# Performance work log

Hardware: AMD Instinct MI355X
Metric: run time of the kernel (lower is better)

## Reference

```python
import jax, jax.numpy as jnp
import numpy as np

BATCH_SIZE = 4
TEMPERATURE = 0.07
NEG_MASK_VAL = -10.0


def setup_inputs() -> dict:
    key = jax.random.key(0)
    k1, k2 = jax.random.split(key)
    N, D = 16384, 256  # N = batch_size * n_patches
    feat_q = jax.random.normal(k1, (N, D), dtype=jnp.float32)
    feat_k = jax.random.normal(k2, (N, D), dtype=jnp.float32)
    return {"feat_q": feat_q, "feat_k": feat_k}


def reference(feat_q, feat_k):
    N, d = feat_q.shape
    feat_k = jax.lax.stop_gradient(feat_k)  # detach
    # positive logits: dot of matching rows -> [N, 1]
    l_pos = jnp.einsum('nd,nd->n', feat_q, feat_k)[:, None]
    q = feat_q.reshape(BATCH_SIZE, -1, d)  # [B, P, D]
    k = feat_k.reshape(BATCH_SIZE, -1, d)
    P = q.shape[1]
    # intra-batch-element negatives: [B, P, P]
    l_neg = jnp.einsum('bpd,bqd->bpq', q, k)
    eye = jnp.eye(P, dtype=bool)[None, :, :]
    l_neg = jnp.where(eye, jnp.float32(NEG_MASK_VAL), l_neg).reshape(-1, P)
    out = jnp.concatenate([l_pos, l_neg], axis=1) / TEMPERATURE  # [N, 1+P]
    # cross-entropy with target class 0, reduction='none'
    loss = -jax.nn.log_softmax(out, axis=1)[:, 0]
    return loss
```

## Files before the change

### kernel.cpp

```cpp
#include <hip/hip_runtime.h>
#include <hip/hip_bf16.h>


typedef __attribute__((ext_vector_type(8))) short short8;
typedef __attribute__((ext_vector_type(4))) float f32x4;

#define BATCH 4
#define PN 4096
#define DD 256
#define NP (BATCH * PN)

constexpr float kLog2e = 1.4426950408889634f;
constexpr float kScale = kLog2e / 0.07f;
constexpr float kMask2 = -10.0f * kScale;
constexpr float kLn2   = 0.6931471805599453f;
constexpr float kNegInf = -3.0e38f;

__device__ __forceinline__ unsigned short f2bf(float f) {
  __hip_bfloat16 h = __float2bfloat16(f);
  return *reinterpret_cast<unsigned short*>(&h);
}

__device__ __forceinline__ float fexp2(float x) {
#if __has_builtin(__builtin_amdgcn_exp2f)
  return __builtin_amdgcn_exp2f(x);
#else
  return exp2f(x);
#endif
}
__device__ __forceinline__ float flog2(float x) {
#if __has_builtin(__builtin_amdgcn_logf)
  return __builtin_amdgcn_logf(x);
#else
  return log2f(x);
#endif
}

__global__ void k_convert(const float* __restrict__ src,
                          unsigned short* __restrict__ dst, int n4) {
  int i = blockIdx.x * blockDim.x + threadIdx.x;
  if (i >= n4) return;
  float4 v = reinterpret_cast<const float4*>(src)[i];
  ushort4 o;
  o.x = f2bf(v.x); o.y = f2bf(v.y); o.z = f2bf(v.z); o.w = f2bf(v.w);
  reinterpret_cast<ushort4*>(dst)[i] = o;
}

__device__ __forceinline__ void stage16(const char* __restrict__ src,
                                        char* ldsbase, int tid) {
  const int wv = tid >> 6;
#pragma unroll
  for (int ip = 0; ip < 4; ip++) {
    const int o   = ip * 4096 + tid * 16;
    const int row = o >> 9;
    const int so  = o ^ ((row & 15) << 4);
    __builtin_amdgcn_global_load_lds(
        (const __attribute__((address_space(1))) void*)(src + so),
        (__attribute__((address_space(3))) void*)(ldsbase + ip * 4096 + wv * 1024),
        16, 0, 0);
  }
}

__device__ __forceinline__ void stage_tile(const char* __restrict__ src,
                                           char* ldsbase, int tid) {
  const int wv = tid >> 6;
#pragma unroll
  for (int ip = 0; ip < 8; ip++) {
    const int o   = ip * 4096 + tid * 16;
    const int row = o >> 9;
    const int so  = o ^ ((row & 15) << 4);
    __builtin_amdgcn_global_load_lds(
        (const __attribute__((address_space(1))) void*)(src + so),
        (__attribute__((address_space(3))) void*)(ldsbase + ip * 4096 + wv * 1024),
        16, 0, 0);
  }
}

__global__ __launch_bounds__(256, 4) void k_nce32(
    const float* __restrict__ fq, const unsigned short* __restrict__ kb,
    float* __restrict__ pl, float* __restrict__ pp) {
  __shared__ __align__(16) char kt[2][32 * 512];

  const int blk = blockIdx.x;
  const int b   = blk & 3;
  const int rt  = (blk >> 2) & 31;
  const int kc  = blk >> 7;
  const int R0  = rt * 128;
  const int C0  = kc * 512;
  const int tid = threadIdx.x;
  const int w   = tid >> 6;
  const int l   = tid & 63;
  const int g   = l >> 4;
  const int li  = l & 15;

  const char* ksrc = reinterpret_cast<const char*>(kb) +
                     ((size_t)b * PN + C0) * 512;

  stage16(ksrc, kt[0], tid);

  short8 a[2][8];
#pragma unroll
  for (int af = 0; af < 2; af++) {
    const float* qrow =
        fq + ((size_t)(b * PN + R0 + w * 32 + af * 16 + li)) * DD;
#pragma unroll
    for (int ks = 0; ks < 8; ks++) {
      const float* p = qrow + ks * 32 + g * 8;
      float4 v0 = *reinterpret_cast<const float4*>(p);
      float4 v1 = *reinterpret_cast<const float4*>(p + 4);
      a[af][ks][0] = (short)f2bf(v0.x * kScale);
      a[af][ks][1] = (short)f2bf(v0.y * kScale);
      a[af][ks][2] = (short)f2bf(v0.z * kScale);
      a[af][ks][3] = (short)f2bf(v0.w * kScale);
      a[af][ks][4] = (short)f2bf(v1.x * kScale);
      a[af][ks][5] = (short)f2bf(v1.y * kScale);
      a[af][ks][6] = (short)f2bf(v1.z * kScale);
      a[af][ks][7] = (short)f2bf(v1.w * kScale);
    }
  }

  float m[2][4], lsum[2][4];
#pragma unroll
  for (int af = 0; af < 2; af++)
#pragma unroll
    for (int r = 0; r < 4; r++) { m[af][r] = kNegInf; lsum[af][r] = 0.f; }

  const int ctd = (kc == (rt >> 2)) ? ((rt & 3) * 4 + w) : -1;

  __syncthreads();

  for (int ct = 0; ct < 16; ct++) {
    const int cur = ct & 1;
    if (ct + 1 < 16) stage16(ksrc + (size_t)(ct + 1) * 16384, kt[cur ^ 1], tid);

    const char* lb = kt[cur];
    f32x4 acc[2][2];
#pragma unroll
    for (int af = 0; af < 2; af++)
#pragma unroll
      for (int cf = 0; cf < 2; cf++) acc[af][cf] = f32x4{0.f, 0.f, 0.f, 0.f};

#pragma unroll
    for (int ks = 0; ks < 8; ks++) {
#pragma unroll
      for (int cf = 0; cf < 2; cf++) {
        const int row = cf * 16 + li;
        const int off = row * 512 + ((ks * 64 + g * 16) ^ ((row & 15) << 4));
        short8 bf = *reinterpret_cast<const short8*>(lb + off);
        acc[0][cf] = __builtin_amdgcn_mfma_f32_16x16x32_bf16(a[0][ks], bf,
                                                             acc[0][cf], 0, 0, 0);
        acc[1][cf] = __builtin_amdgcn_mfma_f32_16x16x32_bf16(a[1][ks], bf,
                                                             acc[1][cf], 0, 0, 0);
      }
    }

    if (ct == ctd) {
#pragma unroll
      for (int af = 0; af < 2; af++)
#pragma unroll
        for (int r = 0; r < 4; r++)
          if (li == g * 4 + r) {
            pp[b * PN + R0 + w * 32 + af * 16 + g * 4 + r] = acc[af][af][r];
            acc[af][af][r] = kMask2;
          }
    }

#pragma unroll
    for (int af = 0; af < 2; af++)
#pragma unroll
      for (int r = 0; r < 4; r++) {
        float v0 = acc[af][0][r], v1 = acc[af][1][r];
        float t0 = fmaxf(v0, v1);
        float mo = m[af][r];
        float mn = fmaxf(mo, t0);
        lsum[af][r] = lsum[af][r] * fexp2(mo - mn) + fexp2(v0 - mn) + fexp2(v1 - mn);
        m[af][r] = mn;
      }
    __syncthreads();
  }

#pragma unroll
  for (int af = 0; af < 2; af++)
#pragma unroll
    for (int r = 0; r < 4; r++) {
      float m_ = m[af][r], l_ = lsum[af][r];
#pragma unroll
      for (int off = 1; off < 16; off <<= 1) {
        float mo = __shfl_xor(m_, off, 64);
        float lo = __shfl_xor(l_, off, 64);
        float mn = fmaxf(m_, mo);
        l_ = l_ * fexp2(m_ - mn) + lo * fexp2(mo - mn);
        m_ = mn;
      }
      if (li == 0) {
        const int rowg = b * PN + R0 + w * 32 + af * 16 + g * 4 + r;
        pl[kc * NP + rowg] = m_ + flog2(l_);
      }
    }
}

template <int NC>
__global__ void k_combine(const float* __restrict__ pl,
                          const float* __restrict__ pp,
                          float* __restrict__ out) {
  const int i = blockIdx.x * blockDim.x + threadIdx.x;
  if (i >= NP) return;
  float mm = kNegInf;
  float v[NC];
#pragma unroll
  for (int c = 0; c < NC; c++) { v[c] = pl[c * NP + i]; mm = fmaxf(mm, v[c]); }
  float s = 0.f;
#pragma unroll
  for (int c = 0; c < NC; c++) s += fexp2(v[c] - mm);
  float lse = mm + flog2(s);
  float p = pp[i];
  float mn = fmaxf(lse, p);
  float la = mn + flog2(fexp2(lse - mn) + fexp2(p - mn));
  out[i] = (la - p) * kLn2;
}

__global__ __launch_bounds__(256, 2) void k_nce_split(
    const float* __restrict__ fq, const unsigned short* __restrict__ kb,
    float* __restrict__ pl, float* __restrict__ pp) {
  __shared__ __align__(16) char kt[2][64 * 512];
  const int blk = blockIdx.x;
  const int b   = blk & 3;
  const int rt  = (blk >> 2) & 31;
  const int kc  = blk >> 7;
  const int R0  = rt * 128;
  const int tid = threadIdx.x;
  const int w   = tid >> 6;
  const int l   = tid & 63;
  const int g   = l >> 4;
  const int li  = l & 15;

  short8 a[2][8];
#pragma unroll
  for (int af = 0; af < 2; af++) {
    const float* qrow = fq + ((size_t)(b * PN + R0 + w * 32 + af * 16 + li)) * DD;
#pragma unroll
    for (int ks = 0; ks < 8; ks++) {
      const float* p = qrow + ks * 32 + g * 8;
      float4 v0 = *reinterpret_cast<const float4*>(p);
      float4 v1 = *reinterpret_cast<const float4*>(p + 4);
      a[af][ks][0] = (short)f2bf(v0.x * kScale); a[af][ks][1] = (short)f2bf(v0.y * kScale);
      a[af][ks][2] = (short)f2bf(v0.z * kScale); a[af][ks][3] = (short)f2bf(v0.w * kScale);
      a[af][ks][4] = (short)f2bf(v1.x * kScale); a[af][ks][5] = (short)f2bf(v1.y * kScale);
      a[af][ks][6] = (short)f2bf(v1.z * kScale); a[af][ks][7] = (short)f2bf(v1.w * kScale);
    }
  }
  float m[2][4], lsum[2][4], pos[2][4];
#pragma unroll
  for (int af = 0; af < 2; af++)
#pragma unroll
    for (int r = 0; r < 4; r++) { m[af][r] = kNegInf; lsum[af][r] = 0.f; pos[af][r] = kNegInf; }

  const char* ksrc = reinterpret_cast<const char*>(kb) +
                     (size_t)b * PN * 512 + (size_t)kc * 16 * 32768;
  const int diag_gt = (R0 + w * 32) >> 6;
  stage_tile(ksrc, kt[0], tid);
  __syncthreads();
  for (int ct = 0; ct < 16; ct++) {
    const int cur = ct & 1;
    if (ct + 1 < 16) stage_tile(ksrc + (size_t)(ct + 1) * 32768, kt[cur ^ 1], tid);
    const char* lb = kt[cur];
    f32x4 acc[2][4];
#pragma unroll
    for (int af = 0; af < 2; af++)
#pragma unroll
      for (int cf = 0; cf < 4; cf++) acc[af][cf] = f32x4{0.f, 0.f, 0.f, 0.f};
#pragma unroll
    for (int ks = 0; ks < 8; ks++) {
#pragma unroll
      for (int cf = 0; cf < 4; cf++) {
        const int row = cf * 16 + li;
        const int off = row * 512 + ((ks * 64 + g * 16) ^ ((row & 15) << 4));
        short8 bf = *reinterpret_cast<const short8*>(lb + off);
        acc[0][cf] = __builtin_amdgcn_mfma_f32_16x16x32_bf16(a[0][ks], bf, acc[0][cf], 0, 0, 0);
        acc[1][cf] = __builtin_amdgcn_mfma_f32_16x16x32_bf16(a[1][ks], bf, acc[1][cf], 0, 0, 0);
      }
    }
    const int gt = kc * 16 + ct;
    if (gt == diag_gt) {
#pragma unroll
      for (int af = 0; af < 2; af++) {
        const int cfd = ((w & 1) << 1) + af;
#pragma unroll
        for (int cf = 0; cf < 4; cf++)
          if (cf == cfd) {
#pragma unroll
            for (int r = 0; r < 4; r++)
              if (li == g * 4 + r) { pos[af][r] = acc[af][cf][r]; acc[af][cf][r] = kMask2; }
          }
      }
    }
#pragma unroll
    for (int af = 0; af < 2; af++)
#pragma unroll
      for (int r = 0; r < 4; r++) {
        float v0 = acc[af][0][r], v1 = acc[af][1][r];
        float v2 = acc[af][2][r], v3 = acc[af][3][r];
        float t0 = fmaxf(fmaxf(v0, v1), fmaxf(v2, v3));
        float mo = m[af][r];
        float mn = fmaxf(mo, t0);
        float s = fexp2(v0 - mn) + fexp2(v1 - mn) + fexp2(v2 - mn) + fexp2(v3 - mn);
        lsum[af][r] = lsum[af][r] * fexp2(mo - mn) + s;
        m[af][r] = mn;
      }
    __syncthreads();
  }
  const bool diag_chunk = (kc == (rt >> 3));
#pragma unroll
  for (int af = 0; af < 2; af++)
#pragma unroll
    for (int r = 0; r < 4; r++) {
      float m_ = m[af][r], l_ = lsum[af][r], p_ = pos[af][r];
#pragma unroll
      for (int off = 1; off < 16; off <<= 1) {
        float mo = __shfl_xor(m_, off, 64);
        float lo = __shfl_xor(l_, off, 64);
        float po = __shfl_xor(p_, off, 64);
        float mn = fmaxf(m_, mo);
        l_ = l_ * fexp2(m_ - mn) + lo * fexp2(mo - mn);
        m_ = mn;
        p_ = fmaxf(p_, po);
      }
      if (li == 0) {
        const int rowg = b * PN + R0 + w * 32 + af * 16 + g * 4 + r;
        pl[kc * NP + rowg] = m_ + flog2(l_);
        if (diag_chunk) pp[rowg] = p_;
      }
    }
}

__global__ __launch_bounds__(256) void k_nce_full(const float* __restrict__ fq,
                                                  const unsigned short* __restrict__ kb,
                                                  float* __restrict__ out) {
  __shared__ __align__(16) char kt[2][64 * 512];
  const int blk = blockIdx.x;
  const int b = blk & 3, rt = blk >> 2;
  const int R0 = rt * 64;
  const int tid = threadIdx.x;
  const int w = tid >> 6, l = tid & 63, g = l >> 4, li = l & 15;

  const float* qrow = fq + ((size_t)(b * PN + R0 + w * 16 + li)) * DD;
  short8 a[8];
#pragma unroll
  for (int ks = 0; ks < 8; ks++) {
    const float* p = qrow + ks * 32 + g * 8;
    float4 v0 = *reinterpret_cast<const float4*>(p);
    float4 v1 = *reinterpret_cast<const float4*>(p + 4);
    a[ks][0] = (short)f2bf(v0.x * kScale); a[ks][1] = (short)f2bf(v0.y * kScale);
    a[ks][2] = (short)f2bf(v0.z * kScale); a[ks][3] = (short)f2bf(v0.w * kScale);
    a[ks][4] = (short)f2bf(v1.x * kScale); a[ks][5] = (short)f2bf(v1.y * kScale);
    a[ks][6] = (short)f2bf(v1.z * kScale); a[ks][7] = (short)f2bf(v1.w * kScale);
  }
  float m[4], lsum[4], pos[4];
#pragma unroll
  for (int r = 0; r < 4; r++) { m[r] = kNegInf; lsum[r] = 0.f; pos[r] = kNegInf; }
  const char* ksrc = reinterpret_cast<const char*>(kb + (size_t)b * PN * DD);
  stage_tile(ksrc, kt[0], tid);
  __syncthreads();
  for (int ct = 0; ct < 64; ct++) {
    const int cur = ct & 1;
    if (ct + 1 < 64) stage_tile(ksrc + (size_t)(ct + 1) * 32768, kt[cur ^ 1], tid);
    const char* lb = kt[cur];
    f32x4 acc[4];
#pragma unroll
    for (int cf = 0; cf < 4; cf++) acc[cf] = f32x4{0.f, 0.f, 0.f, 0.f};
#pragma unroll
    for (int ks = 0; ks < 8; ks++) {
#pragma unroll
      for (int cf = 0; cf < 4; cf++) {
        const int row = cf * 16 + li;
        const int off = row * 512 + ((ks * 64 + g * 16) ^ ((row & 15) << 4));
        short8 bf = *reinterpret_cast<const short8*>(lb + off);
        acc[cf] = __builtin_amdgcn_mfma_f32_16x16x32_bf16(a[ks], bf, acc[cf], 0, 0, 0);
      }
    }
    if (ct == rt) {
#pragma unroll
      for (int cf = 0; cf < 4; cf++)
        if (cf == w) {
#pragma unroll
          for (int r = 0; r < 4; r++)
            if (li == g * 4 + r) { pos[r] = acc[cf][r]; acc[cf][r] = kMask2; }
        }
    }
#pragma unroll
    for (int r = 0; r < 4; r++) {
      float t0 = fmaxf(fmaxf(acc[0][r], acc[1][r]), fmaxf(acc[2][r], acc[3][r]));
      float mo = m[r];
      float mn = fmaxf(mo, t0);
      float s = fexp2(acc[0][r] - mn) + fexp2(acc[1][r] - mn) +
                fexp2(acc[2][r] - mn) + fexp2(acc[3][r] - mn);
      lsum[r] = lsum[r] * fexp2(mo - mn) + s;
      m[r] = mn;
    }
    __syncthreads();
  }
#pragma unroll
  for (int r = 0; r < 4; r++) {
    float m_ = m[r], l_ = lsum[r], p_ = pos[r];
#pragma unroll
    for (int off = 1; off < 16; off <<= 1) {
      float mo = __shfl_xor(m_, off, 64);
      float lo = __shfl_xor(l_, off, 64);
      float po = __shfl_xor(p_, off, 64);
      float mn = fmaxf(m_, mo);
      l_ = l_ * fexp2(m_ - mn) + lo * fexp2(mo - mn);
      m_ = mn;
      p_ = fmaxf(p_, po);
    }
    float mn  = fmaxf(m_, p_);
    float lse = mn + flog2(l_ * fexp2(m_ - mn) + fexp2(p_ - mn));
    if (li == 0) out[b * PN + R0 + w * 16 + g * 4 + r] = (lse - p_) * kLn2;
  }
}

extern "C" void kernel_launch(void* const* d_in, const int* in_sizes, int n_in,
                              void* d_out, int out_size, void* d_ws, size_t ws_size,
                              hipStream_t stream) {
  const float* fq = (const float*)d_in[0];
  const float* fk = (const float*)d_in[1];
  float* out = (float*)d_out;
  unsigned short* kb = (unsigned short*)d_ws;
  const size_t kbBytes = (size_t)NP * DD * 2;
  const size_t ppBytes = (size_t)NP * 4;
  const size_t pl8Bytes = (size_t)8 * NP * 4;
  const size_t pl4Bytes = (size_t)4 * NP * 4;

  const int n4 = (NP * DD) / 4;
  hipLaunchKernelGGL(k_convert, dim3(n4 / 256), dim3(256), 0, stream, fk, kb, n4);

  if (ws_size >= kbBytes + pl8Bytes + ppBytes) {
    float* pl = (float*)((char*)d_ws + kbBytes);
    float* pp = (float*)((char*)d_ws + kbBytes + pl8Bytes);
    hipLaunchKernelGGL(k_nce32, dim3(1024), dim3(256), 0, stream, fq, kb, pl, pp);
    hipLaunchKernelGGL(k_combine<8>, dim3(NP / 256), dim3(256), 0, stream, pl, pp, out);
  } else if (ws_size >= kbBytes + pl4Bytes + ppBytes) {
    float* pl = (float*)((char*)d_ws + kbBytes);
    float* pp = (float*)((char*)d_ws + kbBytes + pl4Bytes);
    hipLaunchKernelGGL(k_nce_split, dim3(512), dim3(256), 0, stream, fq, kb, pl, pp);
    hipLaunchKernelGGL(k_combine<4>, dim3(NP / 256), dim3(256), 0, stream, pl, pp, out);
  } else {
    hipLaunchKernelGGL(k_nce_full, dim3(BATCH * (PN / 64)), dim3(256), 0, stream,
                       fq, kb, out);
  }
}
```

Measured before the change: 63.16 us.

## Double row tile to 256 per block so each staged key tile is reused more

The main kernel now gives each block 256 query rows instead of 128, with 64 rows per wave and four A fragments held in registers. Each LDS-staged key tile therefore feeds twice as many MFMAs, halving key-tile traffic per output. The grid shrinks from 1024 to 512 blocks and occupancy is pinned to 2 waves per EU. The diagonal-masking logic is rewritten for the new tiling, the split-path fallback is dropped and the old k_nce32 is kept but unused. The risk is more register pressure and fewer resident waves to hide staging latency.

After: 63.50 us. No clear change (+0.5%).

```diff
diff --git a/kernel.cpp b/kernel.cpp
--- a/kernel.cpp
+++ b/kernel.cpp
@@ -76,16 +76,18 @@
   }
 }
 
-__global__ __launch_bounds__(256, 4) void k_nce32(
-    const float* __restrict__ fq, const unsigned short* __restrict__ kb,
-    float* __restrict__ pl, float* __restrict__ pp) {
+__global__ __launch_bounds__(256)
+__attribute__((amdgpu_waves_per_eu(2, 2)))
+void k_nce256(const float* __restrict__ fq, const unsigned short* __restrict__ kb,
+              float* __restrict__ pl, float* __restrict__ pp) {
   __shared__ __align__(16) char kt[2][32 * 512];
 
   const int blk = blockIdx.x;
   const int b   = blk & 3;
-  const int rt  = (blk >> 2) & 31;
-  const int kc  = blk >> 7;
-  const int R0  = rt * 128;
+  const int r2  = blk >> 2;
+  const int rt  = r2 & 15;
+  const int kc  = r2 >> 4;
+  const int R0  = rt * 256;
   const int C0  = kc * 512;
   const int tid = threadIdx.x;
   const int w   = tid >> 6;
@@ -98,11 +100,11 @@
 
   stage16(ksrc, kt[0], tid);
 
-  short8 a[2][8];
-#pragma unroll
-  for (int af = 0; af < 2; af++) {
+  short8 a[4][8];
+#pragma unroll
+  for (int af = 0; af < 4; af++) {
     const float* qrow =
-        fq + ((size_t)(b * PN + R0 + w * 32 + af * 16 + li)) * DD;
+        fq + ((size_t)(b * PN + R0 + w * 64 + af * 16 + li)) * DD;
 #pragma unroll
     for (int ks = 0; ks < 8; ks++) {
       const float* p = qrow + ks * 32 + g * 8;
@@ -119,13 +121,11 @@
     }
   }
 
-  float m[2][4], lsum[2][4];
-#pragma unroll
-  for (int af = 0; af < 2; af++)
+  float m[4][4], lsum[4][4];
+#pragma unroll
+  for (int af = 0; af < 4; af++)
 #pragma unroll
     for (int r = 0; r < 4; r++) { m[af][r] = kNegInf; lsum[af][r] = 0.f; }
-
-  const int ctd = (kc == (rt >> 2)) ? ((rt & 3) * 4 + w) : -1;
 
   __syncthreads();
 
@@ -134,9 +134,9 @@
     if (ct + 1 < 16) stage16(ksrc + (size_t)(ct + 1) * 16384, kt[cur ^ 1], tid);
 
     const char* lb = kt[cur];
-    f32x4 acc[2][2];
-#pragma unroll
-    for (int af = 0; af < 2; af++)
+    f32x4 acc[4][2];
+#pragma unroll
+    for (int af = 0; af < 4; af++)
 #pragma unroll
       for (int cf = 0; cf < 2; cf++) acc[af][cf] = f32x4{0.f, 0.f, 0.f, 0.f};
 
@@ -147,26 +147,37 @@
         const int row = cf * 16 + li;
         const int off = row * 512 + ((ks * 64 + g * 16) ^ ((row & 15) << 4));
         short8 bf = *reinterpret_cast<const short8*>(lb + off);
-        acc[0][cf] = __builtin_amdgcn_mfma_f32_16x16x32_bf16(a[0][ks], bf,
-                                                             acc[0][cf], 0, 0, 0);
-        acc[1][cf] = __builtin_amdgcn_mfma_f32_16x16x32_bf16(a[1][ks], bf,
-                                                             acc[1][cf], 0, 0, 0);
-      }
-    }
-
-    if (ct == ctd) {
-#pragma unroll
-      for (int af = 0; af < 2; af++)
-#pragma unroll
-        for (int r = 0; r < 4; r++)
-          if (li == g * 4 + r) {
-            pp[b * PN + R0 + w * 32 + af * 16 + g * 4 + r] = acc[af][af][r];
-            acc[af][af][r] = kMask2;
-          }
-    }
-
-#pragma unroll
-    for (int af = 0; af < 2; af++)
+#pragma unroll
+        for (int af = 0; af < 4; af++)
+          acc[af][cf] = __builtin_amdgcn_mfma_f32_16x16x32_bf16(a[af][ks], bf,
+                                                                acc[af][cf], 0, 0, 0);
+      }
+    }
+
+#pragma unroll
+    for (int af = 0; af < 4; af++) {
+      const int G = rt * 16 + w * 4 + af;
+      if ((G >> 5) == kc && ct == ((G >> 1) - kc * 16)) {
+        if ((G & 1) == 0) {
+#pragma unroll
+          for (int r = 0; r < 4; r++)
+            if (li == g * 4 + r) {
+              pp[b * PN + R0 + w * 64 + af * 16 + g * 4 + r] = acc[af][0][r];
+              acc[af][0][r] = kMask2;
+            }
+        } else {
+#pragma unroll
+          for (int r = 0; r < 4; r++)
+            if (li == g * 4 + r) {
+              pp[b * PN + R0 + w * 64 + af * 16 + g * 4 + r] = acc[af][1][r];
+              acc[af][1][r] = kMask2;
+            }
+        }
+      }
+    }
+
+#pragma unroll
+    for (int af = 0; af < 4; af++)
 #pragma unroll
       for (int r = 0; r < 4; r++) {
         float v0 = acc[af][0][r], v1 = acc[af][1][r];
@@ -180,7 +191,7 @@
   }
 
 #pragma unroll
-  for (int af = 0; af < 2; af++)
+  for (int af = 0; af < 4; af++)
 #pragma unroll
     for (int r = 0; r < 4; r++) {
       float m_ = m[af][r], l_ = lsum[af][r];
@@ -193,7 +204,7 @@
         m_ = mn;
       }
       if (li == 0) {
-        const int rowg = b * PN + R0 + w * 32 + af * 16 + g * 4 + r;
+        const int rowg = b * PN + R0 + w * 64 + af * 16 + g * 4 + r;
         pl[kc * NP + rowg] = m_ + flog2(l_);
       }
     }
@@ -219,20 +230,26 @@
   out[i] = (la - p) * kLn2;
 }
 
-__global__ __launch_bounds__(256, 2) void k_nce_split(
+__global__ __launch_bounds__(256, 4) void k_nce32(
     const float* __restrict__ fq, const unsigned short* __restrict__ kb,
     float* __restrict__ pl, float* __restrict__ pp) {
-  __shared__ __align__(16) char kt[2][64 * 512];
+  __shared__ __align__(16) char kt[2][32 * 512];
+
   const int blk = blockIdx.x;
   const int b   = blk & 3;
   const int rt  = (blk >> 2) & 31;
   const int kc  = blk >> 7;
   const int R0  = rt * 128;
+  const int C0  = kc * 512;
   const int tid = threadIdx.x;
   const int w   = tid >> 6;
   const int l   = tid & 63;
   const int g   = l >> 4;
   const int li  = l & 15;
+
+  const char* ksrc = reinterpret_cast<const char*>(kb) +
+                     ((size_t)b * PN + C0) * 512;
+  stage16(ksrc, kt[0], tid);
 
   short8 a[2][8];
 #pragma unroll
@@ -249,30 +266,31 @@
       a[af][ks][6] = (short)f2bf(v1.z * kScale); a[af][ks][7] = (short)f2bf(v1.w * kScale);
     }
   }
-  float m[2][4], lsum[2][4], pos[2][4];
+
+  float m[2][4], lsum[2][4];
 #pragma unroll
   for (int af = 0; af < 2; af++)
 #pragma unroll
-    for (int r = 0; r < 4; r++) { m[af][r] = kNegInf; lsum[af][r] = 0.f; pos[af][r] = kNegInf; }
-
-  const char* ksrc = reinterpret_cast<const char*>(kb) +
-                     (size_t)b * PN * 512 + (size_t)kc * 16 * 32768;
-  const int diag_gt = (R0 + w * 32) >> 6;
-  stage_tile(ksrc, kt[0], tid);
+    for (int r = 0; r < 4; r++) { m[af][r] = kNegInf; lsum[af][r] = 0.f; }
+
+  const int ctd = (kc == (rt >> 2)) ? ((rt & 3) * 4 + w) : -1;
   __syncthreads();
+
   for (int ct = 0; ct < 16; ct++) {
     const int cur = ct & 1;
-    if (ct + 1 < 16) stage_tile(ksrc + (size_t)(ct + 1) * 32768, kt[cur ^ 1], tid);
+    if (ct + 1 < 16) stage16(ksrc + (size_t)(ct + 1) * 16384, kt[cur ^ 1], tid);
+
     const char* lb = kt[cur];
-    f32x4 acc[2][4];
+    f32x4 acc[2][2];
 #pragma unroll
     for (int af = 0; af < 2; af++)
 #pragma unroll
-      for (int cf = 0; cf < 4; cf++) acc[af][cf] = f32x4{0.f, 0.f, 0.f, 0.f};
+      for (int cf = 0; cf < 2; cf++) acc[af][cf] = f32x4{0.f, 0.f, 0.f, 0.f};
+
 #pragma unroll
     for (int ks = 0; ks < 8; ks++) {
 #pragma unroll
-      for (int cf = 0; cf < 4; cf++) {
+      for (int cf = 0; cf < 2; cf++) {
         const int row = cf * 16 + li;
         const int off = row * 512 + ((ks * 64 + g * 16) ^ ((row & 15) << 4));
         short8 bf = *reinterpret_cast<const short8*>(lb + off);
@@ -280,55 +298,48 @@
         acc[1][cf] = __builtin_amdgcn_mfma_f32_16x16x32_bf16(a[1][ks], bf, acc[1][cf], 0, 0, 0);
       }
     }
-    const int gt = kc * 16 + ct;
-    if (gt == diag_gt) {
-#pragma unroll
-      for (int af = 0; af < 2; af++) {
-        const int cfd = ((w & 1) << 1) + af;
-#pragma unroll
-        for (int cf = 0; cf < 4; cf++)
-          if (cf == cfd) {
-#pragma unroll
-            for (int r = 0; r < 4; r++)
-              if (li == g * 4 + r) { pos[af][r] = acc[af][cf][r]; acc[af][cf][r] = kMask2; }
+
+    if (ct == ctd) {
+#pragma unroll
+      for (int af = 0; af < 2; af++)
+#pragma unroll
+        for (int r = 0; r < 4; r++)
+          if (li == g * 4 + r) {
+            pp[b * PN + R0 + w * 32 + af * 16 + g * 4 + r] = acc[af][af][r];
+            acc[af][af][r] = kMask2;
           }
-      }
-    }
+    }
+
 #pragma unroll
     for (int af = 0; af < 2; af++)
 #pragma unroll
       for (int r = 0; r < 4; r++) {
         float v0 = acc[af][0][r], v1 = acc[af][1][r];
-        float v2 = acc[af][2][r], v3 = acc[af][3][r];
-        float t0 = fmaxf(fmaxf(v0, v1), fmaxf(v2, v3));
+        float t0 = fmaxf(v0, v1);
         float mo = m[af][r];
         float mn = fmaxf(mo, t0);
-        float s = fexp2(v0 - mn) + fexp2(v1 - mn) + fexp2(v2 - mn) + fexp2(v3 - mn);
-        lsum[af][r] = lsum[af][r] * fexp2(mo - mn) + s;
+        lsum[af][r] = lsum[af][r] * fexp2(mo - mn) + fexp2(v0 - mn) + fexp2(v1 - mn);
         m[af][r] = mn;
       }
     __syncthreads();
   }
-  const bool diag_chunk = (kc == (rt >> 3));
+
 #pragma unroll
   for (int af = 0; af < 2; af++)
 #pragma unroll
     for (int r = 0; r < 4; r++) {
-      float m_ = m[af][r], l_ = lsum[af][r], p_ = pos[af][r];
+      float m_ = m[af][r], l_ = lsum[af][r];
 #pragma unroll
       for (int off = 1; off < 16; off <<= 1) {
         float mo = __shfl_xor(m_, off, 64);
         float lo = __shfl_xor(l_, off, 64);
-        float po = __shfl_xor(p_, off, 64);
         float mn = fmaxf(m_, mo);
         l_ = l_ * fexp2(m_ - mn) + lo * fexp2(mo - mn);
         m_ = mn;
-        p_ = fmaxf(p_, po);
       }
       if (li == 0) {
         const int rowg = b * PN + R0 + w * 32 + af * 16 + g * 4 + r;
         pl[kc * NP + rowg] = m_ + flog2(l_);
-        if (diag_chunk) pp[rowg] = p_;
       }
     }
 }
@@ -428,7 +439,6 @@
   const size_t kbBytes = (size_t)NP * DD * 2;
   const size_t ppBytes = (size_t)NP * 4;
   const size_t pl8Bytes = (size_t)8 * NP * 4;
-  const size_t pl4Bytes = (size_t)4 * NP * 4;
 
   const int n4 = (NP * DD) / 4;
   hipLaunchKernelGGL(k_convert, dim3(n4 / 256), dim3(256), 0, stream, fk, kb, n4);
@@ -436,13 +446,8 @@
   if (ws_size >= kbBytes + pl8Bytes + ppBytes) {
     float* pl = (float*)((char*)d_ws + kbBytes);
     float* pp = (float*)((char*)d_ws + kbBytes + pl8Bytes);
-    hipLaunchKernelGGL(k_nce32, dim3(1024), dim3(256), 0, stream, fq, kb, pl, pp);
+    hipLaunchKernelGGL(k_nce256, dim3(512), dim3(256), 0, stream, fq, kb, pl, pp);
     hipLaunchKernelGGL(k_combine<8>, dim3(NP / 256), dim3(256), 0, stream, pl, pp, out);
-  } else if (ws_size >= kbBytes + pl4Bytes + ppBytes) {
-    float* pl = (float*)((char*)d_ws + kbBytes);
-    float* pp = (float*)((char*)d_ws + kbBytes + pl4Bytes);
-    hipLaunchKernelGGL(k_nce_split, dim3(512), dim3(256), 0, stream, fq, kb, pl, pp);
-    hipLaunchKernelGGL(k_combine<4>, dim3(NP / 256), dim3(256), 0, stream, pl, pp, out);
   } else {
     hipLaunchKernelGGL(k_nce_full, dim3(BATCH * (PN / 64)), dim3(256), 0, stream,
                        fq, kb, out);
```
